# Kernel tuning notes

Measured on AMD Instinct MI355X. Metric: run time of the kernel, lower is better.

## Reference

```python
import jax, jax.numpy as jnp
import numpy as np

E = 2048
H = 16
HD = E // H
S = 2048
B = 2
SCALE = 1.0 / np.sqrt(HD)


def setup_inputs() -> dict:
    key = jax.random.key(0)
    ks = jax.random.split(key, 5)
    std = 1.0 / np.sqrt(E)
    return {
        "inX": jax.random.normal(ks[0], (B, S, E), dtype=jnp.float32),
        "W_qkv": jax.random.normal(ks[1], (E, 3 * E), dtype=jnp.float32) * std,
        "b_qkv": jax.random.normal(ks[2], (3 * E,), dtype=jnp.float32) * std,
        "W_out": jax.random.normal(ks[3], (E, E), dtype=jnp.float32) * std,
        "b_out": jax.random.normal(ks[4], (E,), dtype=jnp.float32) * std,
    }


def reference(inX, W_qkv, b_qkv, W_out, b_out):
    b, s, e = inX.shape
    qkv = inX @ W_qkv + b_qkv                      # [B,S,3E]
    q, k, v = jnp.split(qkv, 3, axis=2)
    # [B,S,H,HD] -> [B,H,S,HD]
    q = q.reshape(b, s, H, HD).transpose(0, 2, 1, 3)
    k = k.reshape(b, s, H, HD).transpose(0, 2, 1, 3)
    v = v.reshape(b, s, H, HD).transpose(0, 2, 1, 3)
    att = jnp.einsum("bhqd,bhkd->bhqk", q, k) * SCALE
    causal = jnp.tril(jnp.ones((s, s), dtype=bool))
    att = jnp.where(causal, att, -jnp.inf)
    att = jax.nn.softmax(att, axis=-1)
    out = jnp.einsum("bhqk,bhkd->bhqd", att, v)
    out = out.transpose(0, 2, 1, 3).reshape(b, s, e)
    return out @ W_out + b_out
```

## Files before the change

kernel.cpp:

```cpp
#include <hip/hip_runtime.h>


typedef unsigned short u16;
typedef unsigned int   u32;
typedef __attribute__((ext_vector_type(4)))  float f32x4;
typedef __attribute__((ext_vector_type(16))) float f32x16;
typedef __attribute__((ext_vector_type(4)))  unsigned int u32x4;
typedef __attribute__((ext_vector_type(4)))  unsigned short u16x4;
typedef __attribute__((ext_vector_type(8)))  short bf16x8;

#define E_    2048
#define H_    16
#define HD_   128
#define S_    2048
#define B_    2
#define M_    (B_ * S_)
#define N1_   (3 * E_)
static constexpr float SCALE = 0.08838834764831845f;
static constexpr float C2LOG = 0.12752224f;

__device__ __forceinline__ u16 f2bf(float f) {
  union { float f; u32 u; } x; x.f = f;
  u32 r = x.u + 0x7fffu + ((x.u >> 16) & 1u);
  return (u16)(r >> 16);
}
__device__ __forceinline__ float bfhi2f(u32 u) {
  union { u32 u; float f; } x; x.u = u & 0xffff0000u; return x.f;
}
__device__ __forceinline__ float bflo2f(u32 u) {
  union { u32 u; float f; } x; x.u = u << 16; return x.f;
}
__device__ __forceinline__ u32 pk2(float a, float b) {
  return (u32)f2bf(a) | ((u32)f2bf(b) << 16);
}

__global__ __launch_bounds__(256) void cvt_bf16(const float* __restrict__ x,
                                                u16* __restrict__ y, int n) {
  int i = (blockIdx.x * 256 + threadIdx.x) * 8;
  if (i >= n) return;
  f32x4 a = *(const f32x4*)(x + i);
  f32x4 b = *(const f32x4*)(x + i + 4);
  u16x4 u0 = { f2bf(a[0]), f2bf(a[1]), f2bf(a[2]), f2bf(a[3]) };
  u16x4 u1 = { f2bf(b[0]), f2bf(b[1]), f2bf(b[2]), f2bf(b[3]) };
  *(u16x4*)(y + i)     = u0;
  *(u16x4*)(y + i + 4) = u1;
}

__global__ __launch_bounds__(256) void transpose_cvt_f32(const float* __restrict__ W,
                                                         u16* __restrict__ Wt,
                                                         int rows, int cols) {
  __shared__ __align__(16) u16 tile[64][68];
  const int ct = blockIdx.x, rt = blockIdx.y;
  const int tid = threadIdx.x;
  const int seg = tid & 15, r0 = tid >> 4;
  for (int p = 0; p < 4; ++p) {
    int r = r0 + p * 16;
    f32x4 f = *(const f32x4*)&W[(size_t)(rt * 64 + r) * cols + ct * 64 + seg * 4];
    u16x4 u = { f2bf(f[0]), f2bf(f[1]), f2bf(f[2]), f2bf(f[3]) };
    *(u16x4*)&tile[r][seg * 4] = u;
  }
  __syncthreads();
  for (int p = 0; p < 4; ++p) {
    int oc = r0 + p * 16;
    u16x4 u = { tile[seg * 4 + 0][oc], tile[seg * 4 + 1][oc],
                tile[seg * 4 + 2][oc], tile[seg * 4 + 3][oc] };
    *(u16x4*)&Wt[(size_t)(ct * 64 + oc) * rows + rt * 64 + seg * 4] = u;
  }
}

__global__ __launch_bounds__(256) void transpose_v(const u16* __restrict__ qkv,
                                                   u16* __restrict__ vt) {
  __shared__ __align__(16) u16 tile[64][68];
  const int st = blockIdx.x;
  const int ct = blockIdx.y;
  const int tid = threadIdx.x;
  const int seg = tid & 15, r0 = tid >> 4;
  for (int p = 0; p < 4; ++p) {
    int r = r0 + p * 16;
    *(u16x4*)&tile[r][seg * 4] =
        *(const u16x4*)&qkv[(size_t)(st * 64 + r) * N1_ + 2 * E_ + ct * 64 + seg * 4];
  }
  __syncthreads();
  const int b = st >> 5, s0 = (st & 31) * 64;
  const int h = ct >> 1, d0 = (ct & 1) * 64;
  for (int p = 0; p < 4; ++p) {
    int oc = r0 + p * 16;
    u16x4 u = { tile[seg * 4 + 0][oc], tile[seg * 4 + 1][oc],
                tile[seg * 4 + 2][oc], tile[seg * 4 + 3][oc] };
    *(u16x4*)&vt[(size_t)((b * H_ + h) * HD_ + d0 + oc) * S_ + s0 + seg * 4] = u;
  }
}

template<int OUT_F32>
__global__ __launch_bounds__(256) void gemm_bt(const u16* __restrict__ A,
                                               const u16* __restrict__ Bt,
                                               const float* __restrict__ bias,
                                               void* __restrict__ Cp,
                                               int M, int N, int K) {
  const int bn = blockIdx.x, bm = blockIdx.y;
  const int tid = threadIdx.x;
  const int wid = tid >> 6, l = tid & 63;
  const int l15 = l & 15, l4 = l >> 4;
  const int wr = wid >> 1, wc = wid & 1;

  __shared__ __align__(16) u16 As[2][128 * 64];
  __shared__ __align__(16) u16 Bs[2][128 * 64];

  f32x4 acc[4][4] = {};

  const int srow  = l >> 3;
  const int sslot = (l & 7) ^ srow;
  const u16* gA = A  + (size_t)(bm * 128 + srow) * K + sslot * 8;
  const u16* gB = Bt + (size_t)(bn * 128 + srow) * K + sslot * 8;

  auto stage = [&](int buf, int kt) {
#pragma unroll
    for (int i = 0; i < 4; ++i) {
      const int rb = i * 32 + wid * 8;
      __builtin_amdgcn_global_load_lds(
          (__attribute__((address_space(1))) const void*)(gA + (size_t)rb * K + kt),
          (__attribute__((address_space(3))) void*)(&As[buf][rb * 64]), 16, 0, 0);
      __builtin_amdgcn_global_load_lds(
          (__attribute__((address_space(1))) const void*)(gB + (size_t)rb * K + kt),
          (__attribute__((address_space(3))) void*)(&Bs[buf][rb * 64]), 16, 0, 0);
    }
  };

  stage(0, 0);
  const int nk = K >> 6;
  for (int n = 0; n < nk; ++n) {
    const int buf = n & 1;
    if (n + 1 < nk) {
      stage(buf ^ 1, (n + 1) << 6);
      asm volatile("s_waitcnt vmcnt(8)" ::: "memory");
    } else {
      asm volatile("s_waitcnt vmcnt(0)" ::: "memory");
    }
    __syncthreads();

#pragma unroll
    for (int ks = 0; ks < 2; ++ks) {
      bf16x8 af[4], bfr[4];
      const int ph = ((ks * 4 + l4) ^ (l15 & 7)) * 8;
#pragma unroll
      for (int i = 0; i < 4; ++i) {
        af[i]  = *(const bf16x8*)&As[buf][(wr * 64 + i * 16 + l15) * 64 + ph];
        bfr[i] = *(const bf16x8*)&Bs[buf][(wc * 64 + i * 16 + l15) * 64 + ph];
      }
      __builtin_amdgcn_s_setprio(1);
#pragma unroll
      for (int mi = 0; mi < 4; ++mi)
#pragma unroll
        for (int ni = 0; ni < 4; ++ni)
          acc[mi][ni] = __builtin_amdgcn_mfma_f32_16x16x32_bf16(af[mi], bfr[ni],
                                                                acc[mi][ni], 0, 0, 0);
      __builtin_amdgcn_s_setprio(0);
    }
    __syncthreads();
  }

  for (int ni = 0; ni < 4; ++ni) {
    int col = bn * 128 + wc * 64 + ni * 16 + l15;
    float bs = bias[col];
    for (int mi = 0; mi < 4; ++mi) {
      int row = bm * 128 + wr * 64 + mi * 16 + l4 * 4;
      for (int j = 0; j < 4; ++j) {
        float v = acc[mi][ni][j] + bs;
        if (OUT_F32) ((float*)Cp)[(size_t)(row + j) * N + col] = v;
        else         ((u16*)Cp)[(size_t)(row + j) * N + col] = f2bf(v);
      }
    }
  }
}

__global__ __launch_bounds__(256) void attn3(const u16* __restrict__ qkv,
                                             const u16* __restrict__ vt,
                                             u16* __restrict__ outp) {
  const int i_lin = (int)blockIdx.x + 16 * (int)blockIdx.y;
  const int bh = i_lin & 31;
  const int h8 = i_lin >> 5;
  const int qt = (h8 < 8) ? h8 : 23 - h8;
  const int b = bh >> 4, h = bh & 15;
  const int tid = threadIdx.x;
  const int w = tid >> 6, l = tid & 63;
  const int l31 = l & 31, hi = l >> 5, l15 = l & 15, l4 = l >> 4;

  __shared__ __align__(16) u16 Ks[128 * 128];
  __shared__ __align__(16) u16 Vs[128 * 128];

  const int q_glob = qt * 128 + w * 32 + l31;
  const int qmin_w = qt * 128 + w * 32;
  const int qmax_w = qmin_w + 31;

  bf16x8 qf[8];
  {
    const u16* qrow = qkv + (size_t)(b * S_ + q_glob) * N1_ + h * HD_;
#pragma unroll
    for (int kd = 0; kd < 8; ++kd) {
      u32x4 raw = *(const u32x4*)(qrow + kd * 16 + hi * 8);
      u32x4 o;
#pragma unroll
      for (int j = 0; j < 4; ++j) {
        float flo = bflo2f(raw[j]) * C2LOG;
        float fhi = bfhi2f(raw[j]) * C2LOG;
        o[j] = (u32)f2bf(flo) | ((u32)f2bf(fhi) << 16);
      }
      union { u32x4 u; bf16x8 b; } cv; cv.u = o; qf[kd] = cv.b;
    }
  }

  int slotKe[8];
#pragma unroll
  for (int kd = 0; kd < 8; ++kd) slotKe[kd] = ((2 * kd + hi) ^ l15) * 8;

  f32x16 o0 = {}, o1 = {}, o2 = {}, o3 = {};
  float m_run = -1e30f, lsum = 0.f;

  const int pairs = qt + 1;
  for (int t = 0; t < pairs; ++t) {
    __syncthreads();
#pragma unroll
    for (int i = 0; i < 8; ++i) {
      const int rowbase = i * 16 + w * 4;
      const int r = rowbase + l4;
      const int e = (l15 ^ (r & 15)) * 8;
      __builtin_amdgcn_global_load_lds(
          (__attribute__((address_space(1))) const void*)
              (qkv + (size_t)(b * S_ + t * 128 + r) * N1_ + E_ + h * HD_ + e),
          (__attribute__((address_space(3))) void*)(Ks + rowbase * 128), 16, 0, 0);
      __builtin_amdgcn_global_load_lds(
          (__attribute__((address_space(1))) const void*)
              (vt + (size_t)(bh * HD_ + r) * S_ + t * 128 + e),
          (__attribute__((address_space(3))) void*)(Vs + rowbase * 128), 16, 0, 0);
    }
    asm volatile("s_waitcnt vmcnt(0)");
    __syncthreads();

#pragma unroll
    for (int p = 0; p < 2; ++p) {
      const int kbase = t * 128 + p * 64;
      if (kbase > qmax_w) continue;

      f32x16 sc0 = {}, sc1 = {};
#pragma unroll
      for (int kd = 0; kd < 8; ++kd) {
        bf16x8 ka0 = *(const bf16x8*)(Ks + (size_t)(p * 64 + l31) * 128 + slotKe[kd]);
        bf16x8 ka1 = *(const bf16x8*)(Ks + (size_t)(p * 64 + 32 + l31) * 128 + slotKe[kd]);
        sc0 = __builtin_amdgcn_mfma_f32_32x32x16_bf16(ka0, qf[kd], sc0, 0, 0, 0);
        sc1 = __builtin_amdgcn_mfma_f32_32x32x16_bf16(ka1, qf[kd], sc1, 0, 0, 0);
      }

      if (kbase + 63 > qmin_w) {
#pragma unroll
        for (int r = 0; r < 16; ++r) {
          int k0 = kbase + 8 * (r >> 2) + 4 * hi + (r & 3);
          if (k0 > q_glob)      sc0[r] = -1e30f;
          if (k0 + 32 > q_glob) sc1[r] = -1e30f;
        }
      }

      float tm = -1e30f;
#pragma unroll
      for (int r = 0; r < 16; ++r) tm = fmaxf(tm, fmaxf(sc0[r], sc1[r]));
      tm = fmaxf(tm, __shfl_xor(tm, 32));
      if (tm > m_run + 8.0f) {
        float alpha = exp2f(m_run - tm);
        m_run = tm;
        lsum *= alpha;
#pragma unroll
        for (int r = 0; r < 16; ++r) {
          o0[r] *= alpha; o1[r] *= alpha; o2[r] *= alpha; o3[r] *= alpha;
        }
      }
      float s0 = 0.f, s1 = 0.f;
#pragma unroll
      for (int r = 0; r < 16; ++r) {
        float p0 = exp2f(sc0[r] - m_run); sc0[r] = p0; s0 += p0;
        float p1 = exp2f(sc1[r] - m_run); sc1[r] = p1; s1 += p1;
      }
      lsum += s0 + s1;

      bf16x8 pf[4];
#pragma unroll
      for (int kd = 0; kd < 4; ++kd) {
        const f32x16& scf = (kd < 2) ? sc0 : sc1;
        const int rb = (kd & 1) * 8;
        u32 xa = pk2(scf[rb + 0], scf[rb + 1]);
        u32 ya = pk2(scf[rb + 2], scf[rb + 3]);
        u32 xb = pk2(scf[rb + 4], scf[rb + 5]);
        u32 yb = pk2(scf[rb + 6], scf[rb + 7]);
        u32 sxa = __shfl_xor(xa, 32), sya = __shfl_xor(ya, 32);
        u32 sxb = __shfl_xor(xb, 32), syb = __shfl_xor(yb, 32);
        u32x4 fw;
        fw[0] = hi ? sxb : xa;   fw[1] = hi ? syb : ya;
        fw[2] = hi ? xb  : sxa;  fw[3] = hi ? yb  : sya;
        union { u32x4 u; bf16x8 b; } cv; cv.u = fw; pf[kd] = cv.b;
      }

#pragma unroll
      for (int kd = 0; kd < 4; ++kd) {
        const int vofs = slotKe[kd] ^ (p * 64);
        bf16x8 va0 = *(const bf16x8*)(Vs + (size_t)(0  + l31) * 128 + vofs);
        bf16x8 va1 = *(const bf16x8*)(Vs + (size_t)(32 + l31) * 128 + vofs);
        bf16x8 va2 = *(const bf16x8*)(Vs + (size_t)(64 + l31) * 128 + vofs);
        bf16x8 va3 = *(const bf16x8*)(Vs + (size_t)(96 + l31) * 128 + vofs);
        o0 = __builtin_amdgcn_mfma_f32_32x32x16_bf16(va0, pf[kd], o0, 0, 0, 0);
        o1 = __builtin_amdgcn_mfma_f32_32x32x16_bf16(va1, pf[kd], o1, 0, 0, 0);
        o2 = __builtin_amdgcn_mfma_f32_32x32x16_bf16(va2, pf[kd], o2, 0, 0, 0);
        o3 = __builtin_amdgcn_mfma_f32_32x32x16_bf16(va3, pf[kd], o3, 0, 0, 0);
      }
    }
  }

  lsum += __shfl_xor(lsum, 32);
  const float inv = 1.0f / lsum;
  u16* orow = outp + (size_t)(b * S_ + q_glob) * E_ + h * HD_;
#pragma unroll
  for (int df = 0; df < 4; ++df) {
    const f32x16& oo = (df == 0) ? o0 : (df == 1) ? o1 : (df == 2) ? o2 : o3;
#pragma unroll
    for (int g = 0; g < 4; ++g) {
      int d = 32 * df + 8 * g + 4 * hi;
      u16x4 u = { f2bf(oo[g * 4 + 0] * inv), f2bf(oo[g * 4 + 1] * inv),
                  f2bf(oo[g * 4 + 2] * inv), f2bf(oo[g * 4 + 3] * inv) };
      *(u16x4*)(orow + d) = u;
    }
  }
}

extern "C" void kernel_launch(void* const* d_in, const int* in_sizes, int n_in,
                              void* d_out, int out_size, void* d_ws, size_t ws_size,
                              hipStream_t stream) {
  const float* inX  = (const float*)d_in[0];
  const float* Wqkv = (const float*)d_in[1];
  const float* bqkv = (const float*)d_in[2];
  const float* Wout = (const float*)d_in[3];
  const float* bout = (const float*)d_in[4];

  char* ws = (char*)d_ws;
  u16* Xb   = (u16*)(ws);
  u16* Wqt  = (u16*)(ws + (16u << 20));
  u16* Wot  = (u16*)(ws + (40u << 20));
  u16* QKV  = (u16*)(ws + (48u << 20));
  u16* Vt   = Wqt;
  u16* Attn = Xb;

  cvt_bf16<<<(M_ * E_) / (256 * 8), 256, 0, stream>>>(inX, Xb, M_ * E_);
  transpose_cvt_f32<<<dim3(N1_ / 64, E_ / 64), 256, 0, stream>>>(Wqkv, Wqt, E_, N1_);
  transpose_cvt_f32<<<dim3(E_ / 64, E_ / 64), 256, 0, stream>>>(Wout, Wot, E_, E_);
  gemm_bt<0><<<dim3(N1_ / 128, M_ / 128), 256, 0, stream>>>(Xb, Wqt, bqkv, (void*)QKV,
                                                            M_, N1_, E_);
  transpose_v<<<dim3(M_ / 64, E_ / 64), 256, 0, stream>>>(QKV, Vt);
  attn3<<<dim3(16, 32), 256, 0, stream>>>(QKV, Vt, Attn);
  gemm_bt<1><<<dim3(E_ / 128, M_ / 128), 256, 0, stream>>>(Attn, Wot, bout, d_out,
                                                           M_, E_, E_);
}
```

Before: 270.4 us.

## Add 256x256-tile 8-wave GEMM with interleaved prefetch for QKV projection

Adds a new GEMM kernel for the QKV projection only. It uses a 256x256 output tile, 512 threads and 128 KB of dynamic LDS, double-buffered. The next K-tile's A and B loads are split into small groups, each issued between the MFMA sub-phases with raw barriers, so global-to-LDS traffic overlaps compute. The larger tile raises operand reuse per LDS load. In exchange the grid shrinks to 384 blocks, which creates wave-quantization and tail risk, and the LDS footprint likely allows only one block per CU.

```diff
diff --git a/kernel.cpp b/kernel.cpp
--- a/kernel.cpp
+++ b/kernel.cpp
@@ -18,6 +18,9 @@
 #define N1_   (3 * E_)
 static constexpr float SCALE = 0.08838834764831845f;
 static constexpr float C2LOG = 0.12752224f;
+
+#define AS1 __attribute__((address_space(1)))
+#define AS3 __attribute__((address_space(3)))
 
 __device__ __forceinline__ u16 f2bf(float f) {
   union { float f; u32 u; } x; x.f = f;
@@ -118,11 +121,11 @@
     for (int i = 0; i < 4; ++i) {
       const int rb = i * 32 + wid * 8;
       __builtin_amdgcn_global_load_lds(
-          (__attribute__((address_space(1))) const void*)(gA + (size_t)rb * K + kt),
-          (__attribute__((address_space(3))) void*)(&As[buf][rb * 64]), 16, 0, 0);
+          (AS1 const void*)(gA + (size_t)rb * K + kt),
+          (AS3 void*)(&As[buf][rb * 64]), 16, 0, 0);
       __builtin_amdgcn_global_load_lds(
-          (__attribute__((address_space(1))) const void*)(gB + (size_t)rb * K + kt),
-          (__attribute__((address_space(3))) void*)(&Bs[buf][rb * 64]), 16, 0, 0);
+          (AS1 const void*)(gB + (size_t)rb * K + kt),
+          (AS3 void*)(&Bs[buf][rb * 64]), 16, 0, 0);
     }
   };
 
@@ -164,6 +167,140 @@
     float bs = bias[col];
     for (int mi = 0; mi < 4; ++mi) {
       int row = bm * 128 + wr * 64 + mi * 16 + l4 * 4;
+      for (int j = 0; j < 4; ++j) {
+        float v = acc[mi][ni][j] + bs;
+        if (OUT_F32) ((float*)Cp)[(size_t)(row + j) * N + col] = v;
+        else         ((u16*)Cp)[(size_t)(row + j) * N + col] = f2bf(v);
+      }
+    }
+  }
+}
+
+template<int OUT_F32>
+__global__ __launch_bounds__(512, 2) void gemm256(const u16* __restrict__ A,
+                                                  const u16* __restrict__ Bt,
+                                                  const float* __restrict__ bias,
+                                                  void* __restrict__ Cp,
+                                                  int M, int N, int K) {
+  extern __shared__ __align__(16) u16 lds[];
+  u16* Asb = lds;
+  u16* Bsb = lds + 2 * 256 * 64;
+
+  const int bn = blockIdx.x, bm = blockIdx.y;
+  const int tid = threadIdx.x;
+  const int wid = tid >> 6, l = tid & 63;
+  const int l15 = l & 15, l4 = l >> 4;
+  const int wr = wid >> 2, wc = wid & 3;
+
+  f32x4 acc[8][4] = {};
+
+  const int srow  = tid >> 3;
+  const int sslot = (tid & 7) ^ (srow & 7);
+  const u16* gA = A  + (size_t)(bm * 256 + srow) * K + sslot * 8;
+  const u16* gB = Bt + (size_t)(bn * 256 + srow) * K + sslot * 8;
+  const int wrb = wid * 8;
+
+  auto issueA = [&](int buf, int kt, int i) {
+    __builtin_amdgcn_global_load_lds(
+        (AS1 const void*)(gA + (size_t)(i * 64) * K + kt),
+        (AS3 void*)(Asb + buf * 16384 + (i * 64 + wrb) * 64), 16, 0, 0);
+  };
+  auto issueB = [&](int buf, int kt, int i) {
+    __builtin_amdgcn_global_load_lds(
+        (AS1 const void*)(gB + (size_t)(i * 64) * K + kt),
+        (AS3 void*)(Bsb + buf * 16384 + (i * 64 + wrb) * 64), 16, 0, 0);
+  };
+
+#pragma unroll
+  for (int i = 0; i < 4; ++i) issueA(0, 0, i);
+#pragma unroll
+  for (int i = 0; i < 4; ++i) issueB(0, 0, i);
+
+  const int nk = K >> 6;
+  for (int n = 0; n < nk; ++n) {
+    const int buf = n & 1;
+    const int kt1 = (n + 1) << 6;
+    const bool more = (n + 1 < nk);
+
+    if (more) {
+      issueA(buf ^ 1, kt1, 0); issueA(buf ^ 1, kt1, 1);
+      asm volatile("s_waitcnt vmcnt(2)" ::: "memory");
+    } else {
+      asm volatile("s_waitcnt vmcnt(0)" ::: "memory");
+    }
+    __builtin_amdgcn_s_barrier();
+
+    const u16* Ab = Asb + buf * 16384 + (size_t)(wr * 128) * 64;
+    const u16* Bb = Bsb + buf * 16384 + (size_t)(wc * 64) * 64;
+    const int ph0 = (l4 ^ (l15 & 7)) * 8;
+    const int ph1 = ((4 + l4) ^ (l15 & 7)) * 8;
+
+    bf16x8 af[4], bfr[4];
+#pragma unroll
+    for (int i = 0; i < 4; ++i) {
+      af[i]  = *(const bf16x8*)(Ab + (size_t)(i * 16 + l15) * 64 + ph0);
+      bfr[i] = *(const bf16x8*)(Bb + (size_t)(i * 16 + l15) * 64 + ph0);
+    }
+    if (more) { issueA(buf ^ 1, kt1, 2); issueA(buf ^ 1, kt1, 3); }
+    __builtin_amdgcn_s_setprio(1);
+#pragma unroll
+    for (int mi = 0; mi < 4; ++mi)
+#pragma unroll
+      for (int ni = 0; ni < 4; ++ni)
+        acc[mi][ni] = __builtin_amdgcn_mfma_f32_16x16x32_bf16(af[mi], bfr[ni],
+                                                              acc[mi][ni], 0, 0, 0);
+    __builtin_amdgcn_s_setprio(0);
+    __builtin_amdgcn_s_barrier();
+
+#pragma unroll
+    for (int i = 0; i < 4; ++i)
+      af[i] = *(const bf16x8*)(Ab + (size_t)(64 + i * 16 + l15) * 64 + ph0);
+    if (more) { issueB(buf ^ 1, kt1, 0); issueB(buf ^ 1, kt1, 1); }
+    __builtin_amdgcn_s_setprio(1);
+#pragma unroll
+    for (int mi = 0; mi < 4; ++mi)
+#pragma unroll
+      for (int ni = 0; ni < 4; ++ni)
+        acc[4 + mi][ni] = __builtin_amdgcn_mfma_f32_16x16x32_bf16(af[mi], bfr[ni],
+                                                                  acc[4 + mi][ni], 0, 0, 0);
+    __builtin_amdgcn_s_setprio(0);
+    __builtin_amdgcn_s_barrier();
+
+#pragma unroll
+    for (int i = 0; i < 4; ++i) {
+      af[i]  = *(const bf16x8*)(Ab + (size_t)(i * 16 + l15) * 64 + ph1);
+      bfr[i] = *(const bf16x8*)(Bb + (size_t)(i * 16 + l15) * 64 + ph1);
+    }
+    if (more) { issueB(buf ^ 1, kt1, 2); issueB(buf ^ 1, kt1, 3); }
+    __builtin_amdgcn_s_setprio(1);
+#pragma unroll
+    for (int mi = 0; mi < 4; ++mi)
+#pragma unroll
+      for (int ni = 0; ni < 4; ++ni)
+        acc[mi][ni] = __builtin_amdgcn_mfma_f32_16x16x32_bf16(af[mi], bfr[ni],
+                                                              acc[mi][ni], 0, 0, 0);
+    __builtin_amdgcn_s_setprio(0);
+    __builtin_amdgcn_s_barrier();
+
+#pragma unroll
+    for (int i = 0; i < 4; ++i)
+      af[i] = *(const bf16x8*)(Ab + (size_t)(64 + i * 16 + l15) * 64 + ph1);
+    __builtin_amdgcn_s_setprio(1);
+#pragma unroll
+    for (int mi = 0; mi < 4; ++mi)
+#pragma unroll
+      for (int ni = 0; ni < 4; ++ni)
+        acc[4 + mi][ni] = __builtin_amdgcn_mfma_f32_16x16x32_bf16(af[mi], bfr[ni],
+                                                                  acc[4 + mi][ni], 0, 0, 0);
+    __builtin_amdgcn_s_setprio(0);
+    __builtin_amdgcn_s_barrier();
+  }
+
+  for (int ni = 0; ni < 4; ++ni) {
+    int col = bn * 256 + wc * 64 + ni * 16 + l15;
+    float bs = bias[col];
+    for (int mi = 0; mi < 8; ++mi) {
+      int row = bm * 256 + wr * 128 + mi * 16 + l4 * 4;
       for (int j = 0; j < 4; ++j) {
         float v = acc[mi][ni][j] + bs;
         if (OUT_F32) ((float*)Cp)[(size_t)(row + j) * N + col] = v;
@@ -225,13 +362,13 @@
       const int r = rowbase + l4;
       const int e = (l15 ^ (r & 15)) * 8;
       __builtin_amdgcn_global_load_lds(
-          (__attribute__((address_space(1))) const void*)
+          (AS1 const void*)
               (qkv + (size_t)(b * S_ + t * 128 + r) * N1_ + E_ + h * HD_ + e),
-          (__attribute__((address_space(3))) void*)(Ks + rowbase * 128), 16, 0, 0);
+          (AS3 void*)(Ks + rowbase * 128), 16, 0, 0);
       __builtin_amdgcn_global_load_lds(
-          (__attribute__((address_space(1))) const void*)
+          (AS1 const void*)
               (vt + (size_t)(bh * HD_ + r) * S_ + t * 128 + e),
-          (__attribute__((address_space(3))) void*)(Vs + rowbase * 128), 16, 0, 0);
+          (AS3 void*)(Vs + rowbase * 128), 16, 0, 0);
     }
     asm volatile("s_waitcnt vmcnt(0)");
     __syncthreads();
@@ -345,11 +482,14 @@
   u16* Vt   = Wqt;
   u16* Attn = Xb;
 
+  (void)hipFuncSetAttribute((const void*)&gemm256<0>,
+                            hipFuncAttributeMaxDynamicSharedMemorySize, 131072);
+
   cvt_bf16<<<(M_ * E_) / (256 * 8), 256, 0, stream>>>(inX, Xb, M_ * E_);
   transpose_cvt_f32<<<dim3(N1_ / 64, E_ / 64), 256, 0, stream>>>(Wqkv, Wqt, E_, N1_);
   transpose_cvt_f32<<<dim3(E_ / 64, E_ / 64), 256, 0, stream>>>(Wout, Wot, E_, E_);
-  gemm_bt<0><<<dim3(N1_ / 128, M_ / 128), 256, 0, stream>>>(Xb, Wqt, bqkv, (void*)QKV,
-                                                            M_, N1_, E_);
+  gemm256<0><<<dim3(N1_ / 256, M_ / 256), 512, 131072, stream>>>(Xb, Wqt, bqkv,
+                                                                 (void*)QKV, M_, N1_, E_);
   transpose_v<<<dim3(M_ / 64, E_ / 64), 256, 0, stream>>>(QKV, Vt);
   attn3<<<dim3(16, 32), 256, 0, stream>>>(QKV, Vt, Attn);
   gemm_bt<1><<<dim3(E_ / 128, M_ / 128), 256, 0, stream>>>(Attn, Wot, bout, d_out,
```

Measured after the change: 278.3 us. 1.03x slower.
